# Optimization experiments

Hardware: AMD Instinct MI355X
Metric: run time of the kernel (lower is better)

The kernel has to match this reference:

```python
import jax, jax.numpy as jnp
import numpy as np

BATCH, IN_DIM, N_HID, OUT_DIM = 8192, 1024, 2048, 256
EDGE_DENSITY = 0.05


def _make_mat():
    # adjacency with activation-type codes: 0=no edge, 1=w*x, 2=relu(w*x), 3=tanh(w*x), 4=sigmoid(w*x)
    rng = np.random.default_rng(0)
    n_rows, n_cols = N_HID + OUT_DIM, IN_DIM + N_HID
    mat = rng.integers(1, 5, size=(n_rows, n_cols)) * (rng.random((n_rows, n_cols)) < EDGE_DENSITY)
    mat[:N_HID, IN_DIM:] = 0  # hidden nodes read only from inputs (valid DAG instance of the loop)
    # guarantee every node has at least one incoming edge (original code assumes this)
    hz = np.where(mat[:N_HID, :IN_DIM].sum(1) == 0)[0]
    mat[hz, hz % IN_DIM] = 1
    oz = np.where(mat[N_HID:].sum(1) == 0)[0]
    mat[N_HID + oz, oz % n_cols] = 1
    return mat.astype(np.int32)


def setup_inputs() -> dict:
    key = jax.random.key(0)
    x = jax.random.normal(key, (BATCH, IN_DIM), dtype=jnp.float32)
    w = jnp.ones((), dtype=jnp.float32)  # constant_weight
    mat = jnp.asarray(_make_mat())
    return {"x": x, "w": w, "mat": mat}


_ACTS = [(1, lambda z: z), (2, jax.nn.relu), (3, jnp.tanh), (4, jax.nn.sigmoid)]


def _node_values(src, w, M):
    # src: [B, S] source node values; M: [R, S] activation-type codes
    # node_r = sum_s act_{M[r,s]}(w * src[:, s]) for M[r,s] != 0
    total = jnp.zeros((src.shape[0], M.shape[0]), dtype=src.dtype)
    ws = w * src
    for t, f in _ACTS:
        mask = (M == t).astype(src.dtype)  # [R, S]
        total = total + f(ws) @ mask.T
    return total


def reference(x, w, mat):
    in_dim = x.shape[1]
    num_hidden = mat.shape[1] - in_dim
    hidden = _node_values(x, w, mat[:num_hidden, :in_dim])          # [B, N_HID]
    src = jnp.concatenate([x, hidden], axis=1)                       # [B, IN+N_HID]
    outputs = _node_values(src, w, mat[num_hidden:, :])              # [B, OUT]
    return outputs
```

## Files before the change

kernel.cpp:

```cpp
#include <hip/hip_runtime.h>
#include <hip/hip_bf16.h>
#include <stdint.h>

#define BATCH   8192
#define IN_DIM  1024
#define N_HID   2048
#define OUT_DIM 256
#define SRC_DIM 3072

#define C     32
#define RB    16
#define BT    256
#define S1_CH (IN_DIM / C)
#define S1_RB (N_HID / RB)
#define S2_CH (SRC_DIM / C)
#define S2_RB (OUT_DIM / RB)
#define NSEG1 (S1_RB * S1_CH)
#define NSEG2 (S2_RB * S2_CH)
#define NCG2  16
#define ZSLOT 128
#define SEG_U32 160
#define ABUF_U32 ((4 * C + 1) * 128)


#define RFL(x) __builtin_amdgcn_readfirstlane((uint32_t)(x))

typedef _Float16 h2 __attribute__((ext_vector_type(2)));

__global__ __launch_bounds__(256) void k_prep(const int* __restrict__ mat,
                       uint32_t* __restrict__ seg1, uint32_t* __restrict__ seg2,
                       uint32_t* __restrict__ hdr1, uint32_t* __restrict__ hdr2) {
    __shared__ uint32_t lseg[4][SEG_U32];
    int wid  = (blockIdx.x * blockDim.x + threadIdx.x) >> 6;
    int wv   = threadIdx.x >> 6;
    int lane = threadIdx.x & 63;
    if (wid >= NSEG1 + NSEG2) return;

    int row0, col0;
    uint32_t *seg, *hdr;
    if (wid < NSEG1) {
        int rb = wid / S1_CH, ch = wid % S1_CH;
        row0 = rb * RB;          col0 = ch * C;
        seg = seg1 + (size_t)wid * SEG_U32;  hdr = hdr1 + wid;
    } else {
        int s  = wid - NSEG1;
        int rb = s / S2_CH, ch = s % S2_CH;
        row0 = N_HID + rb * RB;  col0 = ch * C;
        seg = seg2 + (size_t)s * SEG_U32;    hdr = hdr2 + s;
    }

    uint32_t* ls = lseg[wv];
    for (int k = lane; k < SEG_U32; k += 64) ls[k] = 0x80808080u;
    __asm__ volatile("s_waitcnt lgkmcnt(0)" ::: "memory");
    __builtin_amdgcn_sched_barrier(0);

    int n = 0;
    if (lane < RB) {
        const int4* m4 = (const int4*)(mat + (size_t)(row0 + lane) * SRC_DIM + col0);
        uint8_t* sb = (uint8_t*)ls;
        #pragma unroll
        for (int cc = 0; cc < 8; cc++) {
            int4 q4 = m4[cc];
            int codes[4] = {q4.x, q4.y, q4.z, q4.w};
            #pragma unroll
            for (int k = 0; k < 4; k++) {
                int code = codes[k];
                if (code != 0) {
                    int c = cc * 4 + k;
                    uint8_t slot = (uint8_t)((code - 1) * C + c);
                    if (n == 0) {
                        sb[lane] = slot;
                    } else {
                        int jj = n - 1;
                        int pl = jj >> 1;
                        sb[(size_t)(4 + 9 * pl + 1 + (lane >> 1)) * 4
                           + (lane & 1) * 2 + (jj & 1)] = slot;
                    }
                    n++;
                }
            }
        }
    }
    int m = n;
    #pragma unroll
    for (int d = 1; d < 64; d <<= 1) m = max(m, __shfl_xor(m, d));
    uint32_t Wv = 1u + (uint32_t)(m >> 1);

    for (uint32_t p = 1; p < Wv; p++) {
        unsigned long long b = __ballot(n >= (int)(2 * p));
        if (lane == 0) ls[4 + 9 * (p - 1)] = (uint32_t)(b & 0xFFFFu);
    }
    __asm__ volatile("s_waitcnt lgkmcnt(0)" ::: "memory");
    __builtin_amdgcn_sched_barrier(0);

    for (int k = lane; k < SEG_U32; k += 64) seg[k] = ls[k];
    if (lane == 0) *hdr = Wv;
}

__global__ __launch_bounds__(256) void k_xt(const float* __restrict__ x,
                                            float* __restrict__ x_t) {
    __shared__ float t[64][65];
    const int b0 = blockIdx.x * 64, c0 = blockIdx.y * 64;
    {
        int r  = threadIdx.x >> 4;
        int cq = (threadIdx.x & 15) * 4;
        #pragma unroll
        for (int k = 0; k < 4; k++) {
            int rr = r + 16 * k;
            float4 v = *(const float4*)&x[(size_t)(b0 + rr) * IN_DIM + c0 + cq];
            t[rr][cq + 0] = v.x; t[rr][cq + 1] = v.y;
            t[rr][cq + 2] = v.z; t[rr][cq + 3] = v.w;
        }
    }
    __syncthreads();
    {
        int bq  = (threadIdx.x & 15) * 4;
        int cc0 = threadIdx.x >> 4;
        #pragma unroll
        for (int k = 0; k < 4; k++) {
            int cc = cc0 + 16 * k;
            float4 v;
            v.x = t[bq + 0][cc]; v.y = t[bq + 1][cc];
            v.z = t[bq + 2][cc]; v.w = t[bq + 3][cc];
            *(float4*)&x_t[(size_t)(c0 + cc) * BATCH + b0 + bq] = v;
        }
    }
}

__device__ __forceinline__ uint32_t pkh(float a, float b) {
    auto r = __builtin_amdgcn_cvt_pkrtz(a, b);
    return __builtin_bit_cast(uint32_t, r);
}

__device__ __forceinline__ float rcp_f(float x) { return __builtin_amdgcn_rcpf(x); }

__device__ __forceinline__ void write_acts4(uint32_t* As, int c, int lane, float4 v) {
    *(uint2*)&As[(size_t)(0 * C + c) * 128 + 2 * lane] =
        make_uint2(pkh(v.x, v.y), pkh(v.z, v.w));
    *(uint2*)&As[(size_t)(1 * C + c) * 128 + 2 * lane] =
        make_uint2(pkh(fmaxf(v.x, 0.0f), fmaxf(v.y, 0.0f)),
                   pkh(fmaxf(v.z, 0.0f), fmaxf(v.w, 0.0f)));
    float ex = __expf(-v.x), ey = __expf(-v.y);
    float ez = __expf(-v.z), ew = __expf(-v.w);
    float tx = fmaf(2.0f, rcp_f(fmaf(ex, ex, 1.0f)), -1.0f);
    float ty = fmaf(2.0f, rcp_f(fmaf(ey, ey, 1.0f)), -1.0f);
    float tz = fmaf(2.0f, rcp_f(fmaf(ez, ez, 1.0f)), -1.0f);
    float tw = fmaf(2.0f, rcp_f(fmaf(ew, ew, 1.0f)), -1.0f);
    *(uint2*)&As[(size_t)(2 * C + c) * 128 + 2 * lane] =
        make_uint2(pkh(tx, ty), pkh(tz, tw));
    float sx = rcp_f(1.0f + ex), sy = rcp_f(1.0f + ey);
    float sz = rcp_f(1.0f + ez), sw = rcp_f(1.0f + ew);
    *(uint2*)&As[(size_t)(3 * C + c) * 128 + 2 * lane] =
        make_uint2(pkh(sx, sy), pkh(sz, sw));
}

#define SLOT_ACC(R, S)                                                         \
    {                                                                          \
        uint2 q_ = *(const uint2*)&As[(size_t)(S) * 128 + 2 * lane];           \
        accA[R] += __builtin_bit_cast(h2, q_.x);                               \
        accB[R] += __builtin_bit_cast(h2, q_.y);                               \
    }

#define EDGE_PLANES(SEGBASE, WVAL)                                             \
    {                                                                          \
        const uint32_t* sp_ = (SEGBASE);                                       \
        _Pragma("unroll")                                                      \
        for (int i = 0; i < 4; i++) {                                          \
            uint32_t g = RFL(sp_[i]);                                          \
            SLOT_ACC(4 * i + 0, g & 255u)                                      \
            SLOT_ACC(4 * i + 1, (g >> 8) & 255u)                               \
            SLOT_ACC(4 * i + 2, (g >> 16) & 255u)                              \
            SLOT_ACC(4 * i + 3, g >> 24)                                       \
        }                                                                      \
        _Pragma("unroll 1")                                                    \
        for (uint32_t p = 1; p < (WVAL); p++) {                                \
            const uint32_t* pp_ = sp_ + 4 + 9 * (p - 1);                       \
            uint32_t mask = RFL(pp_[0]);                                       \
            _Pragma("unroll")                                                  \
            for (int r = 0; r < RB; r++) {                                     \
                if (mask & (1u << r)) {                                        \
                    uint32_t h_ = RFL(pp_[1 + (r >> 1)]);                      \
                    uint32_t u_ = (r & 1) ? (h_ >> 16) : h_;                   \
                    SLOT_ACC(r, u_ & 255u)                                     \
                    SLOT_ACC(r, (u_ >> 8) & 255u)                              \
                }                                                              \
            }                                                                  \
        }                                                                      \
    }

__global__ __launch_bounds__(1024, 8) void k_hid(const float* __restrict__ x_t,
                                                 const float* __restrict__ wp,
                                                 const uint32_t* __restrict__ seg1,
                                                 const uint32_t* __restrict__ hdr1,
                                                 uint16_t* __restrict__ hidden_t) {
    __shared__ uint32_t As[ABUF_U32];

    const float w  = wp[0];
    const int tile = blockIdx.x;
    const int cgh  = blockIdx.z;
    const int lane = threadIdx.x & 63;
    const int wv   = __builtin_amdgcn_readfirstlane(threadIdx.x >> 6);
    const int rb   = blockIdx.y * 16 + wv;
    const int b0   = tile * BT;
    const int c0   = cgh * (S1_CH / 2);

    if (threadIdx.x < 128) As[ZSLOT * 128 + threadIdx.x] = 0u;

    h2 accA[RB], accB[RB];
    const h2 hz = {(_Float16)0.0f, (_Float16)0.0f};
    #pragma unroll
    for (int r = 0; r < RB; r++) { accA[r] = hz; accB[r] = hz; }

    float4 v[2];
    #pragma unroll
    for (int j = 0; j < 2; j++) {
        int gcol = c0 * C + wv * 2 + j;
        const float2* xp = (const float2*)&x_t[(size_t)gcol * BATCH + b0];
        float2 u0 = xp[lane], u1 = xp[64 + lane];
        v[j] = make_float4(w * u0.x, w * u0.y, w * u1.x, w * u1.y);
    }

    #pragma unroll 1
    for (int cj = 0; cj < S1_CH / 2; cj++) {
        int ch = c0 + cj;
        __syncthreads();
        write_acts4(As, wv * 2 + 0, lane, v[0]);
        write_acts4(As, wv * 2 + 1, lane, v[1]);
        __syncthreads();
        if (cj + 1 < S1_CH / 2) {
            #pragma unroll
            for (int j = 0; j < 2; j++) {
                int gcol = (ch + 1) * C + wv * 2 + j;
                const float2* xp = (const float2*)&x_t[(size_t)gcol * BATCH + b0];
                float2 u0 = xp[lane], u1 = xp[64 + lane];
                v[j] = make_float4(w * u0.x, w * u0.y, w * u1.x, w * u1.y);
            }
        }
        int sidx = rb * S1_CH + ch;
        uint32_t W = RFL(hdr1[sidx]);
        EDGE_PLANES(seg1 + (size_t)sidx * SEG_U32, W)
    }

    uint16_t* hout = hidden_t + (size_t)cgh * N_HID * BATCH;
    const int row0 = rb * RB;
    #pragma unroll
    for (int r = 0; r < RB; r++) {
        *(uint32_t*)&hout[(size_t)(row0 + r) * BATCH + b0 + 2 * lane] =
            __builtin_bit_cast(uint32_t, accA[r]);
        *(uint32_t*)&hout[(size_t)(row0 + r) * BATCH + b0 + 128 + 2 * lane] =
            __builtin_bit_cast(uint32_t, accB[r]);
    }
}

__device__ __forceinline__ float4 load_src4(const float* __restrict__ x_t,
                                            const uint16_t* __restrict__ hidden_t,
                                            int gcol, int b0, int lane, float w) {
    if (gcol < IN_DIM) {
        const float2* xp = (const float2*)&x_t[(size_t)gcol * BATCH + b0];
        float2 u0 = xp[lane], u1 = xp[64 + lane];
        return make_float4(w * u0.x, w * u0.y, w * u1.x, w * u1.y);
    } else {
        const uint16_t* hp = hidden_t + (size_t)(gcol - IN_DIM) * BATCH + b0;
        const uint16_t* hq = hp + (size_t)N_HID * BATCH;
        uint32_t a0 = *(const uint32_t*)&hp[2 * lane];
        uint32_t a1 = *(const uint32_t*)&hp[128 + 2 * lane];
        uint32_t c0 = *(const uint32_t*)&hq[2 * lane];
        uint32_t c1 = *(const uint32_t*)&hq[128 + 2 * lane];
        h2 s0 = __builtin_bit_cast(h2, a0) + __builtin_bit_cast(h2, c0);
        h2 s1 = __builtin_bit_cast(h2, a1) + __builtin_bit_cast(h2, c1);
        return make_float4(w * (float)s0.x, w * (float)s0.y,
                           w * (float)s1.x, w * (float)s1.y);
    }
}

__global__ __launch_bounds__(1024, 8) void k_out(const float* __restrict__ x_t,
                                                 const uint16_t* __restrict__ hidden_t,
                                                 const float* __restrict__ wp,
                                                 const uint32_t* __restrict__ seg2,
                                                 const uint32_t* __restrict__ hdr2,
                                                 uint32_t* __restrict__ partials) {
    __shared__ uint32_t As[ABUF_U32];

    const float w  = wp[0];
    const int tile = blockIdx.x;
    const int cg   = blockIdx.y;
    const int lane = threadIdx.x & 63;
    const int wv   = __builtin_amdgcn_readfirstlane(threadIdx.x >> 6);
    const int b0   = tile * BT;
    const int nch  = S2_CH / NCG2;

    if (threadIdx.x < 128) As[ZSLOT * 128 + threadIdx.x] = 0u;

    h2 accA[RB], accB[RB];
    const h2 hz = {(_Float16)0.0f, (_Float16)0.0f};
    #pragma unroll
    for (int r = 0; r < RB; r++) { accA[r] = hz; accB[r] = hz; }

    float4 v[2];
    #pragma unroll
    for (int j = 0; j < 2; j++)
        v[j] = load_src4(x_t, hidden_t, (cg * nch) * C + wv * 2 + j, b0, lane, w);

    #pragma unroll 1
    for (int cj = 0; cj < nch; cj++) {
        int ch = cg * nch + cj;
        __syncthreads();
        write_acts4(As, wv * 2 + 0, lane, v[0]);
        write_acts4(As, wv * 2 + 1, lane, v[1]);
        __syncthreads();
        if (cj + 1 < nch) {
            #pragma unroll
            for (int j = 0; j < 2; j++)
                v[j] = load_src4(x_t, hidden_t, (ch + 1) * C + wv * 2 + j, b0, lane, w);
        }
        int sidx = wv * S2_CH + ch;
        uint32_t W = RFL(hdr2[sidx]);
        EDGE_PLANES(seg2 + (size_t)sidx * SEG_U32, W)
    }

    #pragma unroll
    for (int r = 0; r < RB; r++) {
        size_t base = ((size_t)cg * OUT_DIM + wv * RB + r) * (BATCH / 2) + (b0 >> 1);
        partials[base + lane]      = __builtin_bit_cast(uint32_t, accA[r]);
        partials[base + 64 + lane] = __builtin_bit_cast(uint32_t, accB[r]);
    }
}

__global__ __launch_bounds__(256) void k_sum(const uint32_t* __restrict__ partials,
                                             float* __restrict__ out) {
    __shared__ float t[16][130];
    const int b0 = blockIdx.x * 128, r0 = blockIdx.y * 16;
    const int lane = threadIdx.x & 63;
    const int g4   = threadIdx.x >> 6;

    #pragma unroll
    for (int k = 0; k < 4; k++) {
        int rr = g4 * 4 + k;
        float sx = 0.0f, sy = 0.0f;
        #pragma unroll
        for (int cg = 0; cg < NCG2; cg++) {
            uint32_t q = partials[((size_t)cg * OUT_DIM + r0 + rr) * (BATCH / 2)
                                  + (b0 >> 1) + lane];
            h2 h = __builtin_bit_cast(h2, q);
            sx += (float)h.x;
            sy += (float)h.y;
        }
        t[rr][2 * lane]     = sx;
        t[rr][2 * lane + 1] = sy;
    }
    __syncthreads();
    #pragma unroll
    for (int k = 0; k < 2; k++) {
        int idx = threadIdx.x + 256 * k;
        int bb = idx >> 2, rq = idx & 3;
        float4 v;
        v.x = t[rq * 4 + 0][bb];
        v.y = t[rq * 4 + 1][bb];
        v.z = t[rq * 4 + 2][bb];
        v.w = t[rq * 4 + 3][bb];
        *(float4*)&out[(size_t)(b0 + bb) * OUT_DIM + r0 + rq * 4] = v;
    }
}

extern "C" void kernel_launch(void* const* d_in, const int* in_sizes, int n_in,
                              void* d_out, int out_size, void* d_ws, size_t ws_size,
                              hipStream_t stream) {
    const float* x   = (const float*)d_in[0];
    const float* w   = (const float*)d_in[1];
    const int*   mat = (const int*)d_in[2];
    float* out = (float*)d_out;

    uint8_t* ws = (uint8_t*)d_ws;
    size_t off = 0;
    uint16_t* hidden_t = (uint16_t*)(ws + off);
    off += (size_t)2 * BATCH * N_HID * 2;
    float* x_t = (float*)(ws + off);        off += (size_t)IN_DIM * BATCH * 4;
    uint32_t* seg1 = (uint32_t*)(ws + off); off += (size_t)NSEG1 * SEG_U32 * 4;
    uint32_t* seg2 = (uint32_t*)(ws + off); off += (size_t)NSEG2 * SEG_U32 * 4;
    uint32_t* hdr1 = (uint32_t*)(ws + off); off += (size_t)NSEG1 * 4;
    uint32_t* hdr2 = (uint32_t*)(ws + off); off += (size_t)NSEG2 * 4;
    uint32_t* partials = (uint32_t*)(ws + off);
    off += (size_t)NCG2 * OUT_DIM * (BATCH / 2) * 4;
    (void)ws_size; (void)in_sizes; (void)n_in; (void)out_size;

    {
        int nseg = NSEG1 + NSEG2;
        k_prep<<<(nseg + 3) / 4, 256, 0, stream>>>(mat, seg1, seg2, hdr1, hdr2);
    }
    {
        dim3 g(BATCH / 64, IN_DIM / 64);
        k_xt<<<g, 256, 0, stream>>>(x, x_t);
    }
    {
        dim3 g(BATCH / BT, 8, 2);
        k_hid<<<g, 1024, 0, stream>>>(x_t, w, seg1, hdr1, hidden_t);
    }
    {
        dim3 g(BATCH / BT, NCG2);
        k_out<<<g, 1024, 0, stream>>>(x_t, hidden_t, w, seg2, hdr2, partials);
    }
    {
        dim3 g(BATCH / 128, OUT_DIM / 16);
        k_sum<<<g, 256, 0, stream>>>(partials, out);
    }
}
```

Measured before the change: 235.8 us.

## Double-buffer LDS activation planes and drop hidden-layer column split

Both k_hid and k_out now use two LDS activation buffers, so each chunk needs one barrier instead of two and the next chunk's activation writes overlap the current chunk's gather-accumulate. k_hid no longer splits input columns across two z-blocks, which removes the second hidden partial buffer and the extra load-and-add in k_out. The output stage halves its column groups (NCG2 16 to 8), giving fewer partials for k_sum. The cost is twice the LDS per block, occupancy bounds lowered to 4, and half as many blocks for the hidden kernel, so parallelism drops.

After: 262.2 us. 1.11x slower.

```diff
diff --git a/kernel.cpp b/kernel.cpp
--- a/kernel.cpp
+++ b/kernel.cpp
@@ -17,7 +17,7 @@
 #define S2_RB (OUT_DIM / RB)
 #define NSEG1 (S1_RB * S1_CH)
 #define NSEG2 (S2_RB * S2_CH)
-#define NCG2  16
+#define NCG2  8
 #define ZSLOT 128
 #define SEG_U32 160
 #define ABUF_U32 ((4 * C + 1) * 128)
@@ -154,23 +154,23 @@
         make_uint2(pkh(sx, sy), pkh(sz, sw));
 }
 
-#define SLOT_ACC(R, S)                                                         \
+#define SLOT_ACC(AB, R, S)                                                     \
     {                                                                          \
-        uint2 q_ = *(const uint2*)&As[(size_t)(S) * 128 + 2 * lane];           \
+        uint2 q_ = *(const uint2*)&(AB)[(size_t)(S) * 128 + 2 * lane];         \
         accA[R] += __builtin_bit_cast(h2, q_.x);                               \
         accB[R] += __builtin_bit_cast(h2, q_.y);                               \
     }
 
-#define EDGE_PLANES(SEGBASE, WVAL)                                             \
+#define EDGE_PLANES(AB, SEGBASE, WVAL)                                         \
     {                                                                          \
         const uint32_t* sp_ = (SEGBASE);                                       \
         _Pragma("unroll")                                                      \
         for (int i = 0; i < 4; i++) {                                          \
             uint32_t g = RFL(sp_[i]);                                          \
-            SLOT_ACC(4 * i + 0, g & 255u)                                      \
-            SLOT_ACC(4 * i + 1, (g >> 8) & 255u)                               \
-            SLOT_ACC(4 * i + 2, (g >> 16) & 255u)                              \
-            SLOT_ACC(4 * i + 3, g >> 24)                                       \
+            SLOT_ACC(AB, 4 * i + 0, g & 255u)                                  \
+            SLOT_ACC(AB, 4 * i + 1, (g >> 8) & 255u)                           \
+            SLOT_ACC(AB, 4 * i + 2, (g >> 16) & 255u)                          \
+            SLOT_ACC(AB, 4 * i + 3, g >> 24)                                   \
         }                                                                      \
         _Pragma("unroll 1")                                                    \
         for (uint32_t p = 1; p < (WVAL); p++) {                                \
@@ -181,30 +181,31 @@
                 if (mask & (1u << r)) {                                        \
                     uint32_t h_ = RFL(pp_[1 + (r >> 1)]);                      \
                     uint32_t u_ = (r & 1) ? (h_ >> 16) : h_;                   \
-                    SLOT_ACC(r, u_ & 255u)                                     \
-                    SLOT_ACC(r, (u_ >> 8) & 255u)                              \
+                    SLOT_ACC(AB, r, u_ & 255u)                                 \
+                    SLOT_ACC(AB, r, (u_ >> 8) & 255u)                          \
                 }                                                              \
             }                                                                  \
         }                                                                      \
     }
 
-__global__ __launch_bounds__(1024, 8) void k_hid(const float* __restrict__ x_t,
+__global__ __launch_bounds__(1024, 4) void k_hid(const float* __restrict__ x_t,
                                                  const float* __restrict__ wp,
                                                  const uint32_t* __restrict__ seg1,
                                                  const uint32_t* __restrict__ hdr1,
                                                  uint16_t* __restrict__ hidden_t) {
-    __shared__ uint32_t As[ABUF_U32];
+    __shared__ uint32_t As[2 * ABUF_U32];
 
     const float w  = wp[0];
     const int tile = blockIdx.x;
-    const int cgh  = blockIdx.z;
     const int lane = threadIdx.x & 63;
     const int wv   = __builtin_amdgcn_readfirstlane(threadIdx.x >> 6);
     const int rb   = blockIdx.y * 16 + wv;
     const int b0   = tile * BT;
-    const int c0   = cgh * (S1_CH / 2);
-
-    if (threadIdx.x < 128) As[ZSLOT * 128 + threadIdx.x] = 0u;
+
+    if (threadIdx.x < 128) {
+        As[ZSLOT * 128 + threadIdx.x] = 0u;
+        As[ABUF_U32 + ZSLOT * 128 + threadIdx.x] = 0u;
+    }
 
     h2 accA[RB], accB[RB];
     const h2 hz = {(_Float16)0.0f, (_Float16)0.0f};
@@ -214,40 +215,51 @@
     float4 v[2];
     #pragma unroll
     for (int j = 0; j < 2; j++) {
-        int gcol = c0 * C + wv * 2 + j;
+        int gcol = wv * 2 + j;
         const float2* xp = (const float2*)&x_t[(size_t)gcol * BATCH + b0];
         float2 u0 = xp[lane], u1 = xp[64 + lane];
         v[j] = make_float4(w * u0.x, w * u0.y, w * u1.x, w * u1.y);
     }
+    write_acts4(As, wv * 2 + 0, lane, v[0]);
+    write_acts4(As, wv * 2 + 1, lane, v[1]);
+    #pragma unroll
+    for (int j = 0; j < 2; j++) {
+        int gcol = C + wv * 2 + j;
+        const float2* xp = (const float2*)&x_t[(size_t)gcol * BATCH + b0];
+        float2 u0 = xp[lane], u1 = xp[64 + lane];
+        v[j] = make_float4(w * u0.x, w * u0.y, w * u1.x, w * u1.y);
+    }
+    __syncthreads();
 
     #pragma unroll 1
-    for (int cj = 0; cj < S1_CH / 2; cj++) {
-        int ch = c0 + cj;
-        __syncthreads();
-        write_acts4(As, wv * 2 + 0, lane, v[0]);
-        write_acts4(As, wv * 2 + 1, lane, v[1]);
-        __syncthreads();
-        if (cj + 1 < S1_CH / 2) {
-            #pragma unroll
-            for (int j = 0; j < 2; j++) {
-                int gcol = (ch + 1) * C + wv * 2 + j;
-                const float2* xp = (const float2*)&x_t[(size_t)gcol * BATCH + b0];
-                float2 u0 = xp[lane], u1 = xp[64 + lane];
-                v[j] = make_float4(w * u0.x, w * u0.y, w * u1.x, w * u1.y);
+    for (int ch = 0; ch < S1_CH; ch++) {
+        uint32_t* cur = As + (size_t)(ch & 1) * ABUF_U32;
+        uint32_t* nxt = As + (size_t)((ch + 1) & 1) * ABUF_U32;
+        if (ch + 1 < S1_CH) {
+            write_acts4(nxt, wv * 2 + 0, lane, v[0]);
+            write_acts4(nxt, wv * 2 + 1, lane, v[1]);
+            if (ch + 2 < S1_CH) {
+                #pragma unroll
+                for (int j = 0; j < 2; j++) {
+                    int gcol = (ch + 2) * C + wv * 2 + j;
+                    const float2* xp = (const float2*)&x_t[(size_t)gcol * BATCH + b0];
+                    float2 u0 = xp[lane], u1 = xp[64 + lane];
+                    v[j] = make_float4(w * u0.x, w * u0.y, w * u1.x, w * u1.y);
+                }
             }
         }
         int sidx = rb * S1_CH + ch;
         uint32_t W = RFL(hdr1[sidx]);
-        EDGE_PLANES(seg1 + (size_t)sidx * SEG_U32, W)
-    }
-
-    uint16_t* hout = hidden_t + (size_t)cgh * N_HID * BATCH;
+        EDGE_PLANES(cur, seg1 + (size_t)sidx * SEG_U32, W)
+        __syncthreads();
+    }
+
     const int row0 = rb * RB;
     #pragma unroll
     for (int r = 0; r < RB; r++) {
-        *(uint32_t*)&hout[(size_t)(row0 + r) * BATCH + b0 + 2 * lane] =
+        *(uint32_t*)&hidden_t[(size_t)(row0 + r) * BATCH + b0 + 2 * lane] =
             __builtin_bit_cast(uint32_t, accA[r]);
-        *(uint32_t*)&hout[(size_t)(row0 + r) * BATCH + b0 + 128 + 2 * lane] =
+        *(uint32_t*)&hidden_t[(size_t)(row0 + r) * BATCH + b0 + 128 + 2 * lane] =
             __builtin_bit_cast(uint32_t, accB[r]);
     }
 }
@@ -261,25 +273,22 @@
         return make_float4(w * u0.x, w * u0.y, w * u1.x, w * u1.y);
     } else {
         const uint16_t* hp = hidden_t + (size_t)(gcol - IN_DIM) * BATCH + b0;
-        const uint16_t* hq = hp + (size_t)N_HID * BATCH;
         uint32_t a0 = *(const uint32_t*)&hp[2 * lane];
         uint32_t a1 = *(const uint32_t*)&hp[128 + 2 * lane];
-        uint32_t c0 = *(const uint32_t*)&hq[2 * lane];
-        uint32_t c1 = *(const uint32_t*)&hq[128 + 2 * lane];
-        h2 s0 = __builtin_bit_cast(h2, a0) + __builtin_bit_cast(h2, c0);
-        h2 s1 = __builtin_bit_cast(h2, a1) + __builtin_bit_cast(h2, c1);
+        h2 s0 = __builtin_bit_cast(h2, a0);
+        h2 s1 = __builtin_bit_cast(h2, a1);
         return make_float4(w * (float)s0.x, w * (float)s0.y,
                            w * (float)s1.x, w * (float)s1.y);
     }
 }
 
-__global__ __launch_bounds__(1024, 8) void k_out(const float* __restrict__ x_t,
+__global__ __launch_bounds__(1024, 4) void k_out(const float* __restrict__ x_t,
                                                  const uint16_t* __restrict__ hidden_t,
                                                  const float* __restrict__ wp,
                                                  const uint32_t* __restrict__ seg2,
                                                  const uint32_t* __restrict__ hdr2,
                                                  uint32_t* __restrict__ partials) {
-    __shared__ uint32_t As[ABUF_U32];
+    __shared__ uint32_t As[2 * ABUF_U32];
 
     const float w  = wp[0];
     const int tile = blockIdx.x;
@@ -289,7 +298,10 @@
     const int b0   = tile * BT;
     const int nch  = S2_CH / NCG2;
 
-    if (threadIdx.x < 128) As[ZSLOT * 128 + threadIdx.x] = 0u;
+    if (threadIdx.x < 128) {
+        As[ZSLOT * 128 + threadIdx.x] = 0u;
+        As[ABUF_U32 + ZSLOT * 128 + threadIdx.x] = 0u;
+    }
 
     h2 accA[RB], accB[RB];
     const h2 hz = {(_Float16)0.0f, (_Float16)0.0f};
@@ -300,22 +312,31 @@
     #pragma unroll
     for (int j = 0; j < 2; j++)
         v[j] = load_src4(x_t, hidden_t, (cg * nch) * C + wv * 2 + j, b0, lane, w);
+    write_acts4(As, wv * 2 + 0, lane, v[0]);
+    write_acts4(As, wv * 2 + 1, lane, v[1]);
+    #pragma unroll
+    for (int j = 0; j < 2; j++)
+        v[j] = load_src4(x_t, hidden_t, (cg * nch + 1) * C + wv * 2 + j, b0, lane, w);
+    __syncthreads();
 
     #pragma unroll 1
     for (int cj = 0; cj < nch; cj++) {
         int ch = cg * nch + cj;
-        __syncthreads();
-        write_acts4(As, wv * 2 + 0, lane, v[0]);
-        write_acts4(As, wv * 2 + 1, lane, v[1]);
-        __syncthreads();
+        uint32_t* cur = As + (size_t)(cj & 1) * ABUF_U32;
+        uint32_t* nxt = As + (size_t)((cj + 1) & 1) * ABUF_U32;
         if (cj + 1 < nch) {
-            #pragma unroll
-            for (int j = 0; j < 2; j++)
-                v[j] = load_src4(x_t, hidden_t, (ch + 1) * C + wv * 2 + j, b0, lane, w);
+            write_acts4(nxt, wv * 2 + 0, lane, v[0]);
+            write_acts4(nxt, wv * 2 + 1, lane, v[1]);
+            if (cj + 2 < nch) {
+                #pragma unroll
+                for (int j = 0; j < 2; j++)
+                    v[j] = load_src4(x_t, hidden_t, (ch + 2) * C + wv * 2 + j, b0, lane, w);
+            }
         }
         int sidx = wv * S2_CH + ch;
         uint32_t W = RFL(hdr2[sidx]);
-        EDGE_PLANES(seg2 + (size_t)sidx * SEG_U32, W)
+        EDGE_PLANES(cur, seg2 + (size_t)sidx * SEG_U32, W)
+        __syncthreads();
     }
 
     #pragma unroll
@@ -373,7 +394,7 @@
     uint8_t* ws = (uint8_t*)d_ws;
     size_t off = 0;
     uint16_t* hidden_t = (uint16_t*)(ws + off);
-    off += (size_t)2 * BATCH * N_HID * 2;
+    off += (size_t)BATCH * N_HID * 2;
     float* x_t = (float*)(ws + off);        off += (size_t)IN_DIM * BATCH * 4;
     uint32_t* seg1 = (uint32_t*)(ws + off); off += (size_t)NSEG1 * SEG_U32 * 4;
     uint32_t* seg2 = (uint32_t*)(ws + off); off += (size_t)NSEG2 * SEG_U32 * 4;
@@ -392,7 +413,7 @@
         k_xt<<<g, 256, 0, stream>>>(x, x_t);
     }
     {
-        dim3 g(BATCH / BT, 8, 2);
+        dim3 g(BATCH / BT, 8);
         k_hid<<<g, 1024, 0, stream>>>(x_t, w, seg1, hdr1, hidden_t);
     }
     {
```

## Store transposed input as fp16 and reduce output partials with packed fp16 atomics

Applied to the files above, without the earlier changes.

The transpose kernel now folds the weight scale into x and writes it as packed fp16, which halves the transposed-input traffic read by both the hidden and output kernels. The output kernel no longer writes 16 per-chunk-group partial buffers. It accumulates straight into a single fp16 output buffer using global_atomic_pk_add_f16, and the final kernel only converts and transposes that buffer. This removes the large partials write/read, but adds a memset, atomic contention across 16 groups, and more fp16 rounding from the atomic summation and the fp16 input.

Measured after the change: 255.9 us. 8.5% more time.

```diff
diff --git a/kernel.cpp b/kernel.cpp
--- a/kernel.cpp
+++ b/kernel.cpp
@@ -97,9 +97,16 @@
     if (lane == 0) *hdr = Wv;
 }
 
+__device__ __forceinline__ uint32_t pkh(float a, float b) {
+    auto r = __builtin_amdgcn_cvt_pkrtz(a, b);
+    return __builtin_bit_cast(uint32_t, r);
+}
+
 __global__ __launch_bounds__(256) void k_xt(const float* __restrict__ x,
-                                            float* __restrict__ x_t) {
+                                            const float* __restrict__ wp,
+                                            uint16_t* __restrict__ x_h) {
     __shared__ float t[64][65];
+    const float w = wp[0];
     const int b0 = blockIdx.x * 64, c0 = blockIdx.y * 64;
     {
         int r  = threadIdx.x >> 4;
@@ -119,17 +126,12 @@
         #pragma unroll
         for (int k = 0; k < 4; k++) {
             int cc = cc0 + 16 * k;
-            float4 v;
-            v.x = t[bq + 0][cc]; v.y = t[bq + 1][cc];
-            v.z = t[bq + 2][cc]; v.w = t[bq + 3][cc];
-            *(float4*)&x_t[(size_t)(c0 + cc) * BATCH + b0 + bq] = v;
+            float a = w * t[bq + 0][cc], b = w * t[bq + 1][cc];
+            float c = w * t[bq + 2][cc], d = w * t[bq + 3][cc];
+            *(uint2*)&x_h[(size_t)(c0 + cc) * BATCH + b0 + bq] =
+                make_uint2(pkh(a, b), pkh(c, d));
         }
     }
-}
-
-__device__ __forceinline__ uint32_t pkh(float a, float b) {
-    auto r = __builtin_amdgcn_cvt_pkrtz(a, b);
-    return __builtin_bit_cast(uint32_t, r);
 }
 
 __device__ __forceinline__ float rcp_f(float x) { return __builtin_amdgcn_rcpf(x); }
@@ -152,6 +154,14 @@
     float sz = rcp_f(1.0f + ez), sw = rcp_f(1.0f + ew);
     *(uint2*)&As[(size_t)(3 * C + c) * 128 + 2 * lane] =
         make_uint2(pkh(sx, sy), pkh(sz, sw));
+}
+
+__device__ __forceinline__ float4 load_xh4(const uint16_t* __restrict__ x_h,
+                                           int gcol, int b0, int lane) {
+    const uint16_t* xp = x_h + (size_t)gcol * BATCH + b0;
+    h2 a = __builtin_bit_cast(h2, *(const uint32_t*)&xp[2 * lane]);
+    h2 b = __builtin_bit_cast(h2, *(const uint32_t*)&xp[128 + 2 * lane]);
+    return make_float4((float)a.x, (float)a.y, (float)b.x, (float)b.y);
 }
 
 #define SLOT_ACC(R, S)                                                         \
@@ -188,14 +198,12 @@
         }                                                                      \
     }
 
-__global__ __launch_bounds__(1024, 8) void k_hid(const float* __restrict__ x_t,
-                                                 const float* __restrict__ wp,
+__global__ __launch_bounds__(1024, 8) void k_hid(const uint16_t* __restrict__ x_h,
                                                  const uint32_t* __restrict__ seg1,
                                                  const uint32_t* __restrict__ hdr1,
                                                  uint16_t* __restrict__ hidden_t) {
     __shared__ uint32_t As[ABUF_U32];
 
-    const float w  = wp[0];
     const int tile = blockIdx.x;
     const int cgh  = blockIdx.z;
     const int lane = threadIdx.x & 63;
@@ -213,12 +221,8 @@
 
     float4 v[2];
     #pragma unroll
-    for (int j = 0; j < 2; j++) {
-        int gcol = c0 * C + wv * 2 + j;
-        const float2* xp = (const float2*)&x_t[(size_t)gcol * BATCH + b0];
-        float2 u0 = xp[lane], u1 = xp[64 + lane];
-        v[j] = make_float4(w * u0.x, w * u0.y, w * u1.x, w * u1.y);
-    }
+    for (int j = 0; j < 2; j++)
+        v[j] = load_xh4(x_h, c0 * C + wv * 2 + j, b0, lane);
 
     #pragma unroll 1
     for (int cj = 0; cj < S1_CH / 2; cj++) {
@@ -229,12 +233,8 @@
         __syncthreads();
         if (cj + 1 < S1_CH / 2) {
             #pragma unroll
-            for (int j = 0; j < 2; j++) {
-                int gcol = (ch + 1) * C + wv * 2 + j;
-                const float2* xp = (const float2*)&x_t[(size_t)gcol * BATCH + b0];
-                float2 u0 = xp[lane], u1 = xp[64 + lane];
-                v[j] = make_float4(w * u0.x, w * u0.y, w * u1.x, w * u1.y);
-            }
+            for (int j = 0; j < 2; j++)
+                v[j] = load_xh4(x_h, (ch + 1) * C + wv * 2 + j, b0, lane);
         }
         int sidx = rb * S1_CH + ch;
         uint32_t W = RFL(hdr1[sidx]);
@@ -252,13 +252,11 @@
     }
 }
 
-__device__ __forceinline__ float4 load_src4(const float* __restrict__ x_t,
+__device__ __forceinline__ float4 load_src4(const uint16_t* __restrict__ x_h,
                                             const uint16_t* __restrict__ hidden_t,
                                             int gcol, int b0, int lane, float w) {
     if (gcol < IN_DIM) {
-        const float2* xp = (const float2*)&x_t[(size_t)gcol * BATCH + b0];
-        float2 u0 = xp[lane], u1 = xp[64 + lane];
-        return make_float4(w * u0.x, w * u0.y, w * u1.x, w * u1.y);
+        return load_xh4(x_h, gcol, b0, lane);
     } else {
         const uint16_t* hp = hidden_t + (size_t)(gcol - IN_DIM) * BATCH + b0;
         const uint16_t* hq = hp + (size_t)N_HID * BATCH;
@@ -273,12 +271,17 @@
     }
 }
 
-__global__ __launch_bounds__(1024, 8) void k_out(const float* __restrict__ x_t,
+__device__ __forceinline__ void atomic_pk_f16(uint16_t* p, h2 v) {
+    asm volatile("global_atomic_pk_add_f16 %0, %1, off"
+                 :: "v"(p), "v"(__builtin_bit_cast(uint32_t, v)) : "memory");
+}
+
+__global__ __launch_bounds__(1024, 8) void k_out(const uint16_t* __restrict__ x_h,
                                                  const uint16_t* __restrict__ hidden_t,
                                                  const float* __restrict__ wp,
                                                  const uint32_t* __restrict__ seg2,
                                                  const uint32_t* __restrict__ hdr2,
-                                                 uint32_t* __restrict__ partials) {
+                                                 uint16_t* __restrict__ outh) {
     __shared__ uint32_t As[ABUF_U32];
 
     const float w  = wp[0];
@@ -299,7 +302,7 @@
     float4 v[2];
     #pragma unroll
     for (int j = 0; j < 2; j++)
-        v[j] = load_src4(x_t, hidden_t, (cg * nch) * C + wv * 2 + j, b0, lane, w);
+        v[j] = load_src4(x_h, hidden_t, (cg * nch) * C + wv * 2 + j, b0, lane, w);
 
     #pragma unroll 1
     for (int cj = 0; cj < nch; cj++) {
@@ -311,7 +314,7 @@
         if (cj + 1 < nch) {
             #pragma unroll
             for (int j = 0; j < 2; j++)
-                v[j] = load_src4(x_t, hidden_t, (ch + 1) * C + wv * 2 + j, b0, lane, w);
+                v[j] = load_src4(x_h, hidden_t, (ch + 1) * C + wv * 2 + j, b0, lane, w);
         }
         int sidx = wv * S2_CH + ch;
         uint32_t W = RFL(hdr2[sidx]);
@@ -320,13 +323,13 @@
 
     #pragma unroll
     for (int r = 0; r < RB; r++) {
-        size_t base = ((size_t)cg * OUT_DIM + wv * RB + r) * (BATCH / 2) + (b0 >> 1);
-        partials[base + lane]      = __builtin_bit_cast(uint32_t, accA[r]);
-        partials[base + 64 + lane] = __builtin_bit_cast(uint32_t, accB[r]);
-    }
-}
-
-__global__ __launch_bounds__(256) void k_sum(const uint32_t* __restrict__ partials,
+        uint16_t* p = outh + (size_t)(wv * RB + r) * BATCH + b0;
+        atomic_pk_f16(p + 2 * lane,       accA[r]);
+        atomic_pk_f16(p + 128 + 2 * lane, accB[r]);
+    }
+}
+
+__global__ __launch_bounds__(256) void k_fin(const uint16_t* __restrict__ outh,
                                              float* __restrict__ out) {
     __shared__ float t[16][130];
     const int b0 = blockIdx.x * 128, r0 = blockIdx.y * 16;
@@ -336,17 +339,10 @@
     #pragma unroll
     for (int k = 0; k < 4; k++) {
         int rr = g4 * 4 + k;
-        float sx = 0.0f, sy = 0.0f;
-        #pragma unroll
-        for (int cg = 0; cg < NCG2; cg++) {
-            uint32_t q = partials[((size_t)cg * OUT_DIM + r0 + rr) * (BATCH / 2)
-                                  + (b0 >> 1) + lane];
-            h2 h = __builtin_bit_cast(h2, q);
-            sx += (float)h.x;
-            sy += (float)h.y;
-        }
-        t[rr][2 * lane]     = sx;
-        t[rr][2 * lane + 1] = sy;
+        uint32_t q = *(const uint32_t*)&outh[(size_t)(r0 + rr) * BATCH + b0 + 2 * lane];
+        h2 h = __builtin_bit_cast(h2, q);
+        t[rr][2 * lane]     = (float)h.x;
+        t[rr][2 * lane + 1] = (float)h.y;
     }
     __syncthreads();
     #pragma unroll
@@ -374,14 +370,15 @@
     size_t off = 0;
     uint16_t* hidden_t = (uint16_t*)(ws + off);
     off += (size_t)2 * BATCH * N_HID * 2;
-    float* x_t = (float*)(ws + off);        off += (size_t)IN_DIM * BATCH * 4;
+    uint16_t* x_h = (uint16_t*)(ws + off);  off += (size_t)IN_DIM * BATCH * 2;
     uint32_t* seg1 = (uint32_t*)(ws + off); off += (size_t)NSEG1 * SEG_U32 * 4;
     uint32_t* seg2 = (uint32_t*)(ws + off); off += (size_t)NSEG2 * SEG_U32 * 4;
     uint32_t* hdr1 = (uint32_t*)(ws + off); off += (size_t)NSEG1 * 4;
     uint32_t* hdr2 = (uint32_t*)(ws + off); off += (size_t)NSEG2 * 4;
-    uint32_t* partials = (uint32_t*)(ws + off);
-    off += (size_t)NCG2 * OUT_DIM * (BATCH / 2) * 4;
+    uint16_t* outh = (uint16_t*)(ws + off); off += (size_t)OUT_DIM * BATCH * 2;
     (void)ws_size; (void)in_sizes; (void)n_in; (void)out_size;
+
+    hipMemsetAsync(outh, 0, (size_t)OUT_DIM * BATCH * 2, stream);
 
     {
         int nseg = NSEG1 + NSEG2;
@@ -389,18 +386,18 @@
     }
     {
         dim3 g(BATCH / 64, IN_DIM / 64);
-        k_xt<<<g, 256, 0, stream>>>(x, x_t);
+        k_xt<<<g, 256, 0, stream>>>(x, w, x_h);
     }
     {
         dim3 g(BATCH / BT, 8, 2);
-        k_hid<<<g, 1024, 0, stream>>>(x_t, w, seg1, hdr1, hidden_t);
+        k_hid<<<g, 1024, 0, stream>>>(x_h, seg1, hdr1, hidden_t);
     }
     {
         dim3 g(BATCH / BT, NCG2);
-        k_out<<<g, 1024, 0, stream>>>(x_t, hidden_t, w, seg2, hdr2, partials);
+        k_out<<<g, 1024, 0, stream>>>(x_h, hidden_t, w, seg2, hdr2, outh);
     }
     {
         dim3 g(BATCH / 128, OUT_DIM / 16);
-        k_sum<<<g, 256, 0, stream>>>(partials, out);
-    }
-}
+        k_fin<<<g, 256, 0, stream>>>(outh, out);
+    }
+}
```
